# Kernel optimization log

Measured on AMD Instinct MI355X. Metric: run time of the kernel, lower is better.

## Reference

```python
import jax, jax.numpy as jnp
import numpy as np

FEATURES = 64
GROUPS = 8
KH = KW = 3
PAD = 1


def conv2d(x, w):
    # x: [B,C,H,W], w: [O,I,kh,kw], stride 1, padding 1
    return jax.lax.conv_general_dilated(
        x, w, window_strides=(1, 1), padding=((PAD, PAD), (PAD, PAD)),
        dimension_numbers=('NCHW', 'OIHW', 'NCHW'))


def _bilinear_gather(x, ys, xs):
    # x: [B,C,H,W]; ys, xs: [B,K,H,W] float sample coords. Zero outside bounds
    # (torchvision deform_conv2d convention).
    B, C, H, W = x.shape
    xf = x.reshape(B, C, H * W)
    y0 = jnp.floor(ys)
    x0 = jnp.floor(xs)
    dy = ys - y0
    dx = xs - x0

    def corner(yi, xi, w):
        valid = (yi >= 0) & (yi < H) & (xi >= 0) & (xi < W)
        yc = jnp.clip(yi, 0, H - 1).astype(jnp.int32)
        xc = jnp.clip(xi, 0, W - 1).astype(jnp.int32)
        idx = (yc * W + xc).reshape(B, -1)  # [B, K*H*W]
        g = jax.vmap(lambda xb, ib: xb[:, ib])(xf, idx)  # [B,C,K*H*W]
        g = g.reshape(B, C, *ys.shape[1:])  # [B,C,K,H,W]
        wm = jnp.where(valid, w, 0.0).astype(x.dtype)[:, None]
        return g * wm

    return (corner(y0, x0, (1 - dy) * (1 - dx))
            + corner(y0, x0 + 1, (1 - dy) * dx)
            + corner(y0 + 1, x0, dy * (1 - dx))
            + corner(y0 + 1, x0 + 1, dy * dx))


def deform_conv2d(x, offset, weight, bias, groups):
    # x: [B,C,H,W]; offset: [B,2*K,H,W] as (dy,dx) pairs per kernel tap;
    # weight: [Cout, Cin//groups, KH, KW]; bias: [Cout]. stride=1, pad=1, dil=1.
    B, C, H, W = x.shape
    Cout = weight.shape[0]
    K = KH * KW
    ky, kx = jnp.meshgrid(jnp.arange(KH), jnp.arange(KW), indexing='ij')
    ky = ky.reshape(K).astype(x.dtype)
    kx = kx.reshape(K).astype(x.dtype)
    off = offset.reshape(B, K, 2, H, W)
    ys = ((jnp.arange(H, dtype=x.dtype) - PAD)[None, None, :, None]
          + ky[None, :, None, None] + off[:, :, 0])  # [B,K,H,W]
    xs = ((jnp.arange(W, dtype=x.dtype) - PAD)[None, None, None, :]
          + kx[None, :, None, None] + off[:, :, 1])
    patches = _bilinear_gather(x, ys, xs)  # [B,C,K,H,W]
    p = patches.reshape(B, groups, C // groups, K, H, W)
    wg = weight.reshape(groups, Cout // groups, C // groups, K)
    out = jnp.einsum('bgikhw,goik->bgohw', p, wg).reshape(B, Cout, H, W)
    return out + bias[None, :, None, None]


def setup_inputs() -> dict:
    key = jax.random.key(0)
    ks = jax.random.split(key, 7)
    C = FEATURES
    x = jax.random.normal(ks[0], (8, C, 128, 128), dtype=jnp.float32)
    fan = C * KH * KW
    offset_w = jax.random.normal(ks[1], (2 * KH * KW, C, KH, KW), jnp.float32) / np.sqrt(fan)
    offset_b = jax.random.normal(ks[2], (2 * KH * KW,), jnp.float32) * 0.01
    prelu_a = jnp.full((1,), 0.25, dtype=jnp.float32)
    deconv_w = jax.random.normal(ks[3], (C, C // GROUPS, KH, KW), jnp.float32) / np.sqrt((C // GROUPS) * KH * KW)
    deconv_b = jax.random.normal(ks[4], (C,), jnp.float32) * 0.01
    conv_w = jax.random.normal(ks[5], (C, C, KH, KW), jnp.float32) / np.sqrt(fan)
    return {"x": x, "offset_w": offset_w, "offset_b": offset_b,
            "prelu_a": prelu_a, "deconv_w": deconv_w, "deconv_b": deconv_b,
            "conv_w": conv_w}


def reference(x, offset_w, offset_b, prelu_a, deconv_w, deconv_b, conv_w):
    residual = x
    o = conv2d(x, offset_w) + offset_b[None, :, None, None]
    offset = jnp.where(o >= 0, o, prelu_a[0] * o)          # PReLU(offset_conv1(x))
    feat = deform_conv2d(x, offset, deconv_w, deconv_b, GROUPS)
    atten = jax.nn.softmax(conv2d(x, conv_w), axis=-1)     # softmax over W
    return atten * feat + residual
```

## Files before the change

### kernel.cpp

```cpp
#include <hip/hip_runtime.h>
#include <math.h>

#define BB 8
#define C 64
#define H 128
#define W 128
#define KO 18
#define NG 8
#define CPG 8
#define KK 9
#define HW (H * W)
#define NCO 96
#define KTOT 576
#define AROW 72
#define PROW 72

typedef __bf16 bf16x8 __attribute__((ext_vector_type(8)));
typedef float f32x4 __attribute__((ext_vector_type(4)));
typedef unsigned int uint4v __attribute__((ext_vector_type(4)));

static __device__ __forceinline__ unsigned short f2bf(float f) {
    union { float f; unsigned u; } v; v.f = f;
    unsigned r = v.u + 0x7FFFu + ((v.u >> 16) & 1u);
    return (unsigned short)(r >> 16);
}

static __device__ __forceinline__ bf16x8 load_bf8(const unsigned short* p) {
    uint4v u = *(const uint4v*)p;
    return __builtin_bit_cast(bf16x8, u);
}
static __device__ __forceinline__ bf16x8 lds_bf8(const unsigned short* p) {
    uint4v u = *(const uint4v*)p;
    return __builtin_bit_cast(bf16x8, u);
}

static __device__ __forceinline__ float bflo(unsigned u) {
    union { unsigned u; float f; } v; v.u = u << 16; return v.f;
}
static __device__ __forceinline__ float bfhi(unsigned u) {
    union { unsigned u; float f; } v; v.u = u & 0xFFFF0000u; return v.f;
}

__global__ __launch_bounds__(256)
void xcl_prep_kernel(const float* __restrict__ x, unsigned short* __restrict__ xcl)
{
    const int lane = threadIdx.x & 63;
    const int cg = threadIdx.x >> 6;
    const size_t P = (size_t)blockIdx.x * 64 + lane;
    const int b = (int)(P >> 14);
    const int hw = (int)(P & 16383);

    union { unsigned short s[16]; uint4v v[2]; } u;
    const float* xp = x + ((size_t)b * C + cg * 16) * HW + hw;
#pragma unroll
    for (int i = 0; i < 16; i++)
        u.s[i] = f2bf(xp[i * HW]);

    uint4v* dst = (uint4v*)(xcl + P * 64 + cg * 16);
    dst[0] = u.v[0];
    dst[1] = u.v[1];
}

__global__ __launch_bounds__(256)
void wt_prep_kernel(const float* __restrict__ convw,
                    const float* __restrict__ offw,
                    unsigned short* __restrict__ wT)
{
    const int i = blockIdx.x * 256 + threadIdx.x;
    if (i >= NCO * KTOT) return;
    const int k = i % KTOT;
    const int co = i / KTOT;
    const int t = k >> 6;
    const int ci = k & 63;
    float v = 0.f;
    if (co < 64)       v = convw[((size_t)co * C + ci) * KK + t];
    else if (co < 82)  v = offw[((size_t)(co - 64) * C + ci) * KK + t];
    wT[i] = f2bf(v);
}

__global__ __launch_bounds__(256)
void awg_prep_kernel(const float* __restrict__ dw, unsigned short* __restrict__ awg)
{
    const int i = blockIdx.x * 256 + threadIdx.x;
    if (i >= KK * 2 * 32 * 32) return;
    const int ci = i & 31;
    const int row = (i >> 5) & 31;
    const int hf = (i >> 10) & 1;
    const int t = i >> 11;
    const int co = hf * 32 + row;
    const int cig = hf * 32 + ci;
    float v = 0.f;
    if ((co >> 3) == (cig >> 3))
        v = dw[((size_t)co * CPG + (cig & 7)) * KK + t];
    awg[i] = f2bf(v);
}

__global__ __launch_bounds__(256)
void conv_mfma_kernel(const unsigned short* __restrict__ xcl,
                      const unsigned short* __restrict__ wT,
                      const float* __restrict__ offb,
                      const float* __restrict__ prelu_a,
                      float* __restrict__ ws_offset,
                      float* __restrict__ ws_atten)
{
    __shared__ unsigned short aw[NCO * AROW];
    __shared__ float smax[4][2][64];
    __shared__ float ssum[4][2][64];

    const int lane = threadIdx.x & 63;
    const int q = __builtin_amdgcn_readfirstlane(threadIdx.x >> 6);
    const int m = lane & 15;
    const int qq = lane >> 4;
    const int hp = blockIdx.x & 63;
    const int b = blockIdx.x >> 6;
    const int h0 = hp * 2;

    f32x4 acc[4][6];
#pragma unroll
    for (int nt = 0; nt < 4; nt++)
#pragma unroll
        for (int mt = 0; mt < 6; mt++)
            acc[nt][mt] = (f32x4){0.f, 0.f, 0.f, 0.f};

    const int col0 = q * 32 + m;

#pragma unroll
    for (int t = 0; t < KK; t++) {
        const int dy = t / 3 - 1;
        const int dx = t % 3 - 1;

        bf16x8 bfr[2][4];
#pragma unroll
        for (int half = 0; half < 2; half++)
#pragma unroll
            for (int nt = 0; nt < 4; nt++) {
                const int y = h0 + (nt >> 1) + dy;
                const int xx = col0 + (nt & 1) * 16 + dx;
                const bool ok = (y >= 0) && (y < H) && (xx >= 0) && (xx < W);
                bf16x8 v = {};
                if (ok)
                    v = load_bf8(xcl + (((size_t)(b * H + y) * W + xx) * 64
                                        + half * 32 + qq * 8));
                bfr[half][nt] = v;
            }

        __syncthreads();
#pragma unroll
        for (int c = threadIdx.x; c < NCO * 8; c += 256) {
            const int row = c >> 3;
            const int col8 = (c & 7) * 8;
            *(uint4v*)(aw + row * AROW + col8) =
                *(const uint4v*)(wT + (size_t)row * KTOT + t * 64 + col8);
        }
        __syncthreads();

#pragma unroll
        for (int half = 0; half < 2; half++) {
#pragma unroll
            for (int mt = 0; mt < 6; mt++) {
                const bf16x8 afr = lds_bf8(
                    aw + (mt * 16 + m) * AROW + half * 32 + qq * 8);
#pragma unroll
                for (int nt = 0; nt < 4; nt++)
                    acc[nt][mt] = __builtin_amdgcn_mfma_f32_16x16x32_bf16(
                        afr, bfr[half][nt], acc[nt][mt], 0, 0, 0);
            }
        }
    }

    const float a = prelu_a[0];
#pragma unroll
    for (int nt = 0; nt < 4; nt++) {
        const int wrow = h0 + (nt >> 1);
        const int wcol = col0 + (nt & 1) * 16;
#pragma unroll
        for (int r = 0; r < 4; r++) {
            const int j = qq * 4 + r;
            float v = acc[nt][4][r] + offb[j];
            v = (v >= 0.f) ? v : a * v;
            ws_offset[((size_t)(b * KO + j)) * HW + wrow * W + wcol] = v;
        }
#pragma unroll
        for (int r = 0; r < 4; r++) {
            const int j = 16 + qq * 4 + r;
            if (j < KO) {
                float v = acc[nt][5][r] + offb[j];
                v = (v >= 0.f) ? v : a * v;
                ws_offset[((size_t)(b * KO + j)) * HW + wrow * W + wcol] = v;
            }
        }
    }

    float pm[2][4][4];
#pragma unroll
    for (int rr = 0; rr < 2; rr++)
#pragma unroll
        for (int mt = 0; mt < 4; mt++)
#pragma unroll
            for (int r = 0; r < 4; r++)
                pm[rr][mt][r] = fmaxf(acc[rr * 2][mt][r], acc[rr * 2 + 1][mt][r]);
#pragma unroll
    for (int off = 1; off < 16; off <<= 1)
#pragma unroll
        for (int rr = 0; rr < 2; rr++)
#pragma unroll
            for (int mt = 0; mt < 4; mt++)
#pragma unroll
                for (int r = 0; r < 4; r++)
                    pm[rr][mt][r] = fmaxf(pm[rr][mt][r],
                                          __shfl_xor(pm[rr][mt][r], off, 64));
    if (m == 0) {
#pragma unroll
        for (int rr = 0; rr < 2; rr++)
#pragma unroll
            for (int mt = 0; mt < 4; mt++)
#pragma unroll
                for (int r = 0; r < 4; r++)
                    smax[q][rr][mt * 16 + qq * 4 + r] = pm[rr][mt][r];
    }
    __syncthreads();

    float gm[2][4][4];
#pragma unroll
    for (int rr = 0; rr < 2; rr++)
#pragma unroll
        for (int mt = 0; mt < 4; mt++)
#pragma unroll
            for (int r = 0; r < 4; r++) {
                const int co = mt * 16 + qq * 4 + r;
                gm[rr][mt][r] = fmaxf(fmaxf(smax[0][rr][co], smax[1][rr][co]),
                                      fmaxf(smax[2][rr][co], smax[3][rr][co]));
            }
    float ps[2][4][4];
#pragma unroll
    for (int rr = 0; rr < 2; rr++)
#pragma unroll
        for (int mt = 0; mt < 4; mt++)
#pragma unroll
            for (int r = 0; r < 4; r++) {
                acc[rr * 2][mt][r] = __expf(acc[rr * 2][mt][r] - gm[rr][mt][r]);
                acc[rr * 2 + 1][mt][r] = __expf(acc[rr * 2 + 1][mt][r] - gm[rr][mt][r]);
                ps[rr][mt][r] = acc[rr * 2][mt][r] + acc[rr * 2 + 1][mt][r];
            }
#pragma unroll
    for (int off = 1; off < 16; off <<= 1)
#pragma unroll
        for (int rr = 0; rr < 2; rr++)
#pragma unroll
            for (int mt = 0; mt < 4; mt++)
#pragma unroll
                for (int r = 0; r < 4; r++)
                    ps[rr][mt][r] += __shfl_xor(ps[rr][mt][r], off, 64);
    if (m == 0) {
#pragma unroll
        for (int rr = 0; rr < 2; rr++)
#pragma unroll
            for (int mt = 0; mt < 4; mt++)
#pragma unroll
                for (int r = 0; r < 4; r++)
                    ssum[q][rr][mt * 16 + qq * 4 + r] = ps[rr][mt][r];
    }
    __syncthreads();

#pragma unroll
    for (int rr = 0; rr < 2; rr++)
#pragma unroll
        for (int mt = 0; mt < 4; mt++)
#pragma unroll
            for (int r = 0; r < 4; r++) {
                const int co = mt * 16 + qq * 4 + r;
                const float rinv = 1.f / (ssum[0][rr][co] + ssum[1][rr][co]
                                          + ssum[2][rr][co] + ssum[3][rr][co]);
                float* op = ws_atten + ((size_t)(b * 64 + co)) * HW
                            + (h0 + rr) * W;
                op[col0] = acc[rr * 2][mt][r] * rinv;
                op[col0 + 16] = acc[rr * 2 + 1][mt][r] * rinv;
            }
}

__global__ __launch_bounds__(256)
void deform_mfma_kernel(const float* __restrict__ x,
                        const unsigned short* __restrict__ xcl,
                        const unsigned short* __restrict__ awg,
                        const float* __restrict__ db,
                        const float* __restrict__ ws_offset,
                        const float* __restrict__ ws_atten,
                        float* __restrict__ out)
{
    __shared__ unsigned short Pl[4 * 2 * 16 * PROW];

    const int lane = threadIdx.x & 63;
    const int wv = __builtin_amdgcn_readfirstlane(threadIdx.x >> 6);

    const int b = blockIdx.x & 7;
    const int h = (blockIdx.x >> 3) & 127;
    const int halfrow = blockIdx.x >> 10;
    const int w0 = halfrow * 64 + wv * 16;

    const int pA = lane >> 3;
    const int pB = pA + 8;
    const int ch = lane & 7;

    const unsigned short* xclb = xcl + (size_t)b * HW * 64;
    const float* offbase = ws_offset + (size_t)b * KO * HW + h * W + w0;
    unsigned short* const Pw0 = Pl + (wv * 2 + 0) * 16 * PROW;
    unsigned short* const Pw1 = Pl + (wv * 2 + 1) * 16 * PROW;

    f32x4 acc[4];
#pragma unroll
    for (int i = 0; i < 4; i++) acc[i] = (f32x4){0.f, 0.f, 0.f, 0.f};

    float dyA = offbase[pA];
    float dxA = offbase[HW + pA];
    float dyB = offbase[pB];
    float dxB = offbase[HW + pB];

#pragma unroll
    for (int t = 0; t < KK; t++) {
        const int ky = t / 3;
        const int kx = t - ky * 3;

        float ndyA = 0.f, ndxA = 0.f, ndyB = 0.f, ndxB = 0.f;
        if (t + 1 < KK) {
            const float* ob2 = offbase + (size_t)(2 * t + 2) * HW;
            ndyA = ob2[pA];
            ndxA = ob2[HW + pA];
            ndyB = ob2[pB];
            ndxB = ob2[HW + pB];
        }

        float wa[4], wb[4];
        int oa[4], ob[4];
        {
            const float ys = (float)(h - 1 + ky) + dyA;
            const float xs = (float)(w0 + pA - 1 + kx) + dxA;
            const float y0f = floorf(ys), x0f = floorf(xs);
            const int y0 = (int)y0f, x0 = (int)x0f;
            const float fy = ys - y0f, fx = xs - x0f;
            const bool vy0 = (y0 >= 0) & (y0 < H), vy1 = (y0 + 1 >= 0) & (y0 + 1 < H);
            const bool vx0 = (x0 >= 0) & (x0 < W), vx1 = (x0 + 1 >= 0) & (x0 + 1 < W);
            wa[0] = (vy0 && vx0) ? (1.f - fy) * (1.f - fx) : 0.f;
            wa[1] = (vy0 && vx1) ? (1.f - fy) * fx : 0.f;
            wa[2] = (vy1 && vx0) ? fy * (1.f - fx) : 0.f;
            wa[3] = (vy1 && vx1) ? fy * fx : 0.f;
            const int yc0 = min(max(y0, 0), H - 1), yc1 = min(max(y0 + 1, 0), H - 1);
            const int xc0 = min(max(x0, 0), W - 1), xc1 = min(max(x0 + 1, 0), W - 1);
            oa[0] = (yc0 * W + xc0) * 64; oa[1] = (yc0 * W + xc1) * 64;
            oa[2] = (yc1 * W + xc0) * 64; oa[3] = (yc1 * W + xc1) * 64;
        }
        {
            const float ys = (float)(h - 1 + ky) + dyB;
            const float xs = (float)(w0 + pB - 1 + kx) + dxB;
            const float y0f = floorf(ys), x0f = floorf(xs);
            const int y0 = (int)y0f, x0 = (int)x0f;
            const float fy = ys - y0f, fx = xs - x0f;
            const bool vy0 = (y0 >= 0) & (y0 < H), vy1 = (y0 + 1 >= 0) & (y0 + 1 < H);
            const bool vx0 = (x0 >= 0) & (x0 < W), vx1 = (x0 + 1 >= 0) & (x0 + 1 < W);
            wb[0] = (vy0 && vx0) ? (1.f - fy) * (1.f - fx) : 0.f;
            wb[1] = (vy0 && vx1) ? (1.f - fy) * fx : 0.f;
            wb[2] = (vy1 && vx0) ? fy * (1.f - fx) : 0.f;
            wb[3] = (vy1 && vx1) ? fy * fx : 0.f;
            const int yc0 = min(max(y0, 0), H - 1), yc1 = min(max(y0 + 1, 0), H - 1);
            const int xc0 = min(max(x0, 0), W - 1), xc1 = min(max(x0 + 1, 0), W - 1);
            ob[0] = (yc0 * W + xc0) * 64; ob[1] = (yc0 * W + xc1) * 64;
            ob[2] = (yc1 * W + xc0) * 64; ob[3] = (yc1 * W + xc1) * 64;
        }

        uint4v rA[4], rB[4];
#pragma unroll
        for (int c = 0; c < 4; c++) {
            rA[c] = *(const uint4v*)(xclb + oa[c] + ch * 8);
            rB[c] = *(const uint4v*)(xclb + ob[c] + ch * 8);
        }

        unsigned short* const Pwt = (t & 1) ? Pw1 : Pw0;

        {
            bf16x8 pv;
#pragma unroll
            for (int d = 0; d < 4; d++) {
                const float lo = wa[0] * bflo(rA[0][d]) + wa[1] * bflo(rA[1][d])
                               + wa[2] * bflo(rA[2][d]) + wa[3] * bflo(rA[3][d]);
                const float hi = wa[0] * bfhi(rA[0][d]) + wa[1] * bfhi(rA[1][d])
                               + wa[2] * bfhi(rA[2][d]) + wa[3] * bfhi(rA[3][d]);
                pv[2 * d]     = (__bf16)lo;
                pv[2 * d + 1] = (__bf16)hi;
            }
            *(bf16x8*)(Pwt + pA * PROW + ch * 8) = pv;
        }
        {
            bf16x8 pv;
#pragma unroll
            for (int d = 0; d < 4; d++) {
                const float lo = wb[0] * bflo(rB[0][d]) + wb[1] * bflo(rB[1][d])
                               + wb[2] * bflo(rB[2][d]) + wb[3] * bflo(rB[3][d]);
                const float hi = wb[0] * bfhi(rB[0][d]) + wb[1] * bfhi(rB[1][d])
                               + wb[2] * bfhi(rB[2][d]) + wb[3] * bfhi(rB[3][d]);
                pv[2 * d]     = (__bf16)lo;
                pv[2 * d + 1] = (__bf16)hi;
            }
            *(bf16x8*)(Pwt + pB * PROW + ch * 8) = pv;
        }

        asm volatile("s_waitcnt lgkmcnt(0)" ::: "memory");

        const int m = lane & 15;
        const int qq = lane >> 4;
#pragma unroll
        for (int hf = 0; hf < 2; hf++) {
            const bf16x8 bfr = lds_bf8(Pwt + m * PROW + hf * 32 + qq * 8);
#pragma unroll
            for (int mtl = 0; mtl < 2; mtl++) {
                const bf16x8 afr = load_bf8(
                    awg + ((size_t)((t * 2 + hf) * 32 + mtl * 16 + m)) * 32 + qq * 8);
                acc[hf * 2 + mtl] = __builtin_amdgcn_mfma_f32_16x16x32_bf16(
                    afr, bfr, acc[hf * 2 + mtl], 0, 0, 0);
            }
        }

        dyA = ndyA; dxA = ndxA; dyB = ndyB; dxB = ndxB;
    }

    const int n = lane & 15;
    const int qq = lane >> 4;
    const float* attp = ws_atten + (size_t)b * C * HW + h * W + w0 + n;
    const float* xr = x + (size_t)b * C * HW + h * W + w0 + n;
    float* op = out + (size_t)b * C * HW + h * W + w0 + n;
#pragma unroll
    for (int a = 0; a < 4; a++)
#pragma unroll
        for (int r = 0; r < 4; r++) {
            const int co = a * 16 + qq * 4 + r;
            const float f = acc[a][r] + db[co];
            op[(size_t)co * HW] = attp[(size_t)co * HW] * f + xr[(size_t)co * HW];
        }
}

extern "C" void kernel_launch(void* const* d_in, const int* in_sizes, int n_in,
                              void* d_out, int out_size, void* d_ws, size_t ws_size,
                              hipStream_t stream) {
    const float* x        = (const float*)d_in[0];
    const float* offset_w = (const float*)d_in[1];
    const float* offset_b = (const float*)d_in[2];
    const float* prelu_a  = (const float*)d_in[3];
    const float* deconv_w = (const float*)d_in[4];
    const float* deconv_b = (const float*)d_in[5];
    const float* conv_w   = (const float*)d_in[6];
    float* out = (float*)d_out;

    float* ws_offset = (float*)d_ws;
    float* ws_atten  = ws_offset + (size_t)BB * KO * HW;
    unsigned short* xcl = (unsigned short*)(ws_atten + (size_t)BB * C * HW);
    unsigned short* wT  = xcl + (size_t)BB * HW * C;
    unsigned short* awg = wT + (size_t)NCO * KTOT;

    xcl_prep_kernel<<<dim3((BB * HW) / 64), dim3(256), 0, stream>>>(x, xcl);
    wt_prep_kernel<<<dim3((NCO * KTOT + 255) / 256), dim3(256), 0, stream>>>(
        conv_w, offset_w, wT);
    awg_prep_kernel<<<dim3((KK * 2 * 32 * 32 + 255) / 256), dim3(256), 0, stream>>>(
        deconv_w, awg);

    conv_mfma_kernel<<<dim3(BB * H / 2), dim3(256), 0, stream>>>(
        xcl, wT, offset_b, prelu_a, ws_offset, ws_atten);

    deform_mfma_kernel<<<dim3(BB * H * 2), dim3(256), 0, stream>>>(
        x, xcl, awg, deconv_b, ws_offset, ws_atten, out);
}
```

Before: 184.0 us.

## Merge prep kernels into one launch and give conv blocks one row each

The three preprocessing kernels are folded into a single launch that picks its branch by block index, removing two kernel launches. The conv MFMA kernel now handles one output row per block instead of two, doubling the grid to 1024 blocks and halving the accumulator registers. This aims to raise occupancy and parallelism. In exchange, each weight tile copied into LDS is reused over half as many pixels, so weight traffic and barrier overhead per output grow.

```diff
diff --git a/kernel.cpp b/kernel.cpp
--- a/kernel.cpp
+++ b/kernel.cpp
@@ -15,6 +15,10 @@
 #define AROW 72
 #define PROW 72
 
+#define NB_XCL (BB * HW / 64)
+#define NB_WT  (NCO * KTOT / 256)
+#define NB_AWG (KK * 2 * 32 * 32 / 256)
+
 typedef __bf16 bf16x8 __attribute__((ext_vector_type(8)));
 typedef float f32x4 __attribute__((ext_vector_type(4)));
 typedef unsigned int uint4v __attribute__((ext_vector_type(4)));
@@ -42,57 +46,54 @@
 }
 
 __global__ __launch_bounds__(256)
-void xcl_prep_kernel(const float* __restrict__ x, unsigned short* __restrict__ xcl)
+void prep_kernel(const float* __restrict__ x,
+                 const float* __restrict__ convw,
+                 const float* __restrict__ offw,
+                 const float* __restrict__ dw,
+                 unsigned short* __restrict__ xcl,
+                 unsigned short* __restrict__ wT,
+                 unsigned short* __restrict__ awg)
 {
-    const int lane = threadIdx.x & 63;
-    const int cg = threadIdx.x >> 6;
-    const size_t P = (size_t)blockIdx.x * 64 + lane;
-    const int b = (int)(P >> 14);
-    const int hw = (int)(P & 16383);
-
-    union { unsigned short s[16]; uint4v v[2]; } u;
-    const float* xp = x + ((size_t)b * C + cg * 16) * HW + hw;
-#pragma unroll
-    for (int i = 0; i < 16; i++)
-        u.s[i] = f2bf(xp[i * HW]);
-
-    uint4v* dst = (uint4v*)(xcl + P * 64 + cg * 16);
-    dst[0] = u.v[0];
-    dst[1] = u.v[1];
-}
-
-__global__ __launch_bounds__(256)
-void wt_prep_kernel(const float* __restrict__ convw,
-                    const float* __restrict__ offw,
-                    unsigned short* __restrict__ wT)
-{
-    const int i = blockIdx.x * 256 + threadIdx.x;
-    if (i >= NCO * KTOT) return;
-    const int k = i % KTOT;
-    const int co = i / KTOT;
-    const int t = k >> 6;
-    const int ci = k & 63;
-    float v = 0.f;
-    if (co < 64)       v = convw[((size_t)co * C + ci) * KK + t];
-    else if (co < 82)  v = offw[((size_t)(co - 64) * C + ci) * KK + t];
-    wT[i] = f2bf(v);
-}
-
-__global__ __launch_bounds__(256)
-void awg_prep_kernel(const float* __restrict__ dw, unsigned short* __restrict__ awg)
-{
-    const int i = blockIdx.x * 256 + threadIdx.x;
-    if (i >= KK * 2 * 32 * 32) return;
-    const int ci = i & 31;
-    const int row = (i >> 5) & 31;
-    const int hf = (i >> 10) & 1;
-    const int t = i >> 11;
-    const int co = hf * 32 + row;
-    const int cig = hf * 32 + ci;
-    float v = 0.f;
-    if ((co >> 3) == (cig >> 3))
-        v = dw[((size_t)co * CPG + (cig & 7)) * KK + t];
-    awg[i] = f2bf(v);
+    const int blk = blockIdx.x;
+    if (blk < NB_XCL) {
+        const int lane = threadIdx.x & 63;
+        const int cg = threadIdx.x >> 6;
+        const size_t P = (size_t)blk * 64 + lane;
+        const int b = (int)(P >> 14);
+        const int hw = (int)(P & 16383);
+
+        union { unsigned short s[16]; uint4v v[2]; } u;
+        const float* xp = x + ((size_t)b * C + cg * 16) * HW + hw;
+#pragma unroll
+        for (int i = 0; i < 16; i++)
+            u.s[i] = f2bf(xp[i * HW]);
+
+        uint4v* dst = (uint4v*)(xcl + P * 64 + cg * 16);
+        dst[0] = u.v[0];
+        dst[1] = u.v[1];
+    } else if (blk < NB_XCL + NB_WT) {
+        const int i = (blk - NB_XCL) * 256 + threadIdx.x;
+        const int k = i % KTOT;
+        const int co = i / KTOT;
+        const int t = k >> 6;
+        const int ci = k & 63;
+        float v = 0.f;
+        if (co < 64)       v = convw[((size_t)co * C + ci) * KK + t];
+        else if (co < 82)  v = offw[((size_t)(co - 64) * C + ci) * KK + t];
+        wT[i] = f2bf(v);
+    } else {
+        const int i = (blk - NB_XCL - NB_WT) * 256 + threadIdx.x;
+        const int ci = i & 31;
+        const int row = (i >> 5) & 31;
+        const int hf = (i >> 10) & 1;
+        const int t = i >> 11;
+        const int co = hf * 32 + row;
+        const int cig = hf * 32 + ci;
+        float v = 0.f;
+        if ((co >> 3) == (cig >> 3))
+            v = dw[((size_t)co * CPG + (cig & 7)) * KK + t];
+        awg[i] = f2bf(v);
+    }
 }
 
 __global__ __launch_bounds__(256)
@@ -104,20 +105,19 @@
                       float* __restrict__ ws_atten)
 {
     __shared__ unsigned short aw[NCO * AROW];
-    __shared__ float smax[4][2][64];
-    __shared__ float ssum[4][2][64];
+    __shared__ float smax[4][64];
+    __shared__ float ssum[4][64];
 
     const int lane = threadIdx.x & 63;
     const int q = __builtin_amdgcn_readfirstlane(threadIdx.x >> 6);
     const int m = lane & 15;
     const int qq = lane >> 4;
-    const int hp = blockIdx.x & 63;
-    const int b = blockIdx.x >> 6;
-    const int h0 = hp * 2;
-
-    f32x4 acc[4][6];
-#pragma unroll
-    for (int nt = 0; nt < 4; nt++)
+    const int h = blockIdx.x & 127;
+    const int b = blockIdx.x >> 7;
+
+    f32x4 acc[2][6];
+#pragma unroll
+    for (int nt = 0; nt < 2; nt++)
 #pragma unroll
         for (int mt = 0; mt < 6; mt++)
             acc[nt][mt] = (f32x4){0.f, 0.f, 0.f, 0.f};
@@ -129,14 +129,15 @@
         const int dy = t / 3 - 1;
         const int dx = t % 3 - 1;
 
-        bf16x8 bfr[2][4];
+        bf16x8 bfr[2][2];
+        const int y = h + dy;
+        const bool oky = (y >= 0) && (y < H);
 #pragma unroll
         for (int half = 0; half < 2; half++)
 #pragma unroll
-            for (int nt = 0; nt < 4; nt++) {
-                const int y = h0 + (nt >> 1) + dy;
-                const int xx = col0 + (nt & 1) * 16 + dx;
-                const bool ok = (y >= 0) && (y < H) && (xx >= 0) && (xx < W);
+            for (int nt = 0; nt < 2; nt++) {
+                const int xx = col0 + nt * 16 + dx;
+                const bool ok = oky && (xx >= 0) && (xx < W);
                 bf16x8 v = {};
                 if (ok)
                     v = load_bf8(xcl + (((size_t)(b * H + y) * W + xx) * 64
@@ -161,7 +162,7 @@
                 const bf16x8 afr = lds_bf8(
                     aw + (mt * 16 + m) * AROW + half * 32 + qq * 8);
 #pragma unroll
-                for (int nt = 0; nt < 4; nt++)
+                for (int nt = 0; nt < 2; nt++)
                     acc[nt][mt] = __builtin_amdgcn_mfma_f32_16x16x32_bf16(
                         afr, bfr[half][nt], acc[nt][mt], 0, 0, 0);
             }
@@ -170,15 +171,14 @@
 
     const float a = prelu_a[0];
 #pragma unroll
-    for (int nt = 0; nt < 4; nt++) {
-        const int wrow = h0 + (nt >> 1);
-        const int wcol = col0 + (nt & 1) * 16;
+    for (int nt = 0; nt < 2; nt++) {
+        const int wcol = col0 + nt * 16;
 #pragma unroll
         for (int r = 0; r < 4; r++) {
             const int j = qq * 4 + r;
             float v = acc[nt][4][r] + offb[j];
             v = (v >= 0.f) ? v : a * v;
-            ws_offset[((size_t)(b * KO + j)) * HW + wrow * W + wcol] = v;
+            ws_offset[((size_t)(b * KO + j)) * HW + h * W + wcol] = v;
         }
 #pragma unroll
         for (int r = 0; r < 4; r++) {
@@ -186,96 +186,78 @@
             if (j < KO) {
                 float v = acc[nt][5][r] + offb[j];
                 v = (v >= 0.f) ? v : a * v;
-                ws_offset[((size_t)(b * KO + j)) * HW + wrow * W + wcol] = v;
-            }
-        }
-    }
-
-    float pm[2][4][4];
-#pragma unroll
-    for (int rr = 0; rr < 2; rr++)
+                ws_offset[((size_t)(b * KO + j)) * HW + h * W + wcol] = v;
+            }
+        }
+    }
+
+    float pm[4][4];
+#pragma unroll
+    for (int mt = 0; mt < 4; mt++)
+#pragma unroll
+        for (int r = 0; r < 4; r++)
+            pm[mt][r] = fmaxf(acc[0][mt][r], acc[1][mt][r]);
+#pragma unroll
+    for (int off = 1; off < 16; off <<= 1)
 #pragma unroll
         for (int mt = 0; mt < 4; mt++)
 #pragma unroll
             for (int r = 0; r < 4; r++)
-                pm[rr][mt][r] = fmaxf(acc[rr * 2][mt][r], acc[rr * 2 + 1][mt][r]);
+                pm[mt][r] = fmaxf(pm[mt][r], __shfl_xor(pm[mt][r], off, 64));
+    if (m == 0) {
+#pragma unroll
+        for (int mt = 0; mt < 4; mt++)
+#pragma unroll
+            for (int r = 0; r < 4; r++)
+                smax[q][mt * 16 + qq * 4 + r] = pm[mt][r];
+    }
+    __syncthreads();
+
+    float gm[4][4];
+#pragma unroll
+    for (int mt = 0; mt < 4; mt++)
+#pragma unroll
+        for (int r = 0; r < 4; r++) {
+            const int co = mt * 16 + qq * 4 + r;
+            gm[mt][r] = fmaxf(fmaxf(smax[0][co], smax[1][co]),
+                              fmaxf(smax[2][co], smax[3][co]));
+        }
+    float ps[4][4];
+#pragma unroll
+    for (int mt = 0; mt < 4; mt++)
+#pragma unroll
+        for (int r = 0; r < 4; r++) {
+            acc[0][mt][r] = __expf(acc[0][mt][r] - gm[mt][r]);
+            acc[1][mt][r] = __expf(acc[1][mt][r] - gm[mt][r]);
+            ps[mt][r] = acc[0][mt][r] + acc[1][mt][r];
+        }
 #pragma unroll
     for (int off = 1; off < 16; off <<= 1)
 #pragma unroll
-        for (int rr = 0; rr < 2; rr++)
-#pragma unroll
-            for (int mt = 0; mt < 4; mt++)
-#pragma unroll
-                for (int r = 0; r < 4; r++)
-                    pm[rr][mt][r] = fmaxf(pm[rr][mt][r],
-                                          __shfl_xor(pm[rr][mt][r], off, 64));
+        for (int mt = 0; mt < 4; mt++)
+#pragma unroll
+            for (int r = 0; r < 4; r++)
+                ps[mt][r] += __shfl_xor(ps[mt][r], off, 64);
     if (m == 0) {
 #pragma unroll
-        for (int rr = 0; rr < 2; rr++)
-#pragma unroll
-            for (int mt = 0; mt < 4; mt++)
-#pragma unroll
-                for (int r = 0; r < 4; r++)
-                    smax[q][rr][mt * 16 + qq * 4 + r] = pm[rr][mt][r];
+        for (int mt = 0; mt < 4; mt++)
+#pragma unroll
+            for (int r = 0; r < 4; r++)
+                ssum[q][mt * 16 + qq * 4 + r] = ps[mt][r];
     }
     __syncthreads();
 
-    float gm[2][4][4];
-#pragma unroll
-    for (int rr = 0; rr < 2; rr++)
-#pragma unroll
-        for (int mt = 0; mt < 4; mt++)
-#pragma unroll
-            for (int r = 0; r < 4; r++) {
-                const int co = mt * 16 + qq * 4 + r;
-                gm[rr][mt][r] = fmaxf(fmaxf(smax[0][rr][co], smax[1][rr][co]),
-                                      fmaxf(smax[2][rr][co], smax[3][rr][co]));
-            }
-    float ps[2][4][4];
-#pragma unroll
-    for (int rr = 0; rr < 2; rr++)
-#pragma unroll
-        for (int mt = 0; mt < 4; mt++)
-#pragma unroll
-            for (int r = 0; r < 4; r++) {
-                acc[rr * 2][mt][r] = __expf(acc[rr * 2][mt][r] - gm[rr][mt][r]);
-                acc[rr * 2 + 1][mt][r] = __expf(acc[rr * 2 + 1][mt][r] - gm[rr][mt][r]);
-                ps[rr][mt][r] = acc[rr * 2][mt][r] + acc[rr * 2 + 1][mt][r];
-            }
-#pragma unroll
-    for (int off = 1; off < 16; off <<= 1)
-#pragma unroll
-        for (int rr = 0; rr < 2; rr++)
-#pragma unroll
-            for (int mt = 0; mt < 4; mt++)
-#pragma unroll
-                for (int r = 0; r < 4; r++)
-                    ps[rr][mt][r] += __shfl_xor(ps[rr][mt][r], off, 64);
-    if (m == 0) {
-#pragma unroll
-        for (int rr = 0; rr < 2; rr++)
-#pragma unroll
-            for (int mt = 0; mt < 4; mt++)
-#pragma unroll
-                for (int r = 0; r < 4; r++)
-                    ssum[q][rr][mt * 16 + qq * 4 + r] = ps[rr][mt][r];
-    }
-    __syncthreads();
-
-#pragma unroll
-    for (int rr = 0; rr < 2; rr++)
-#pragma unroll
-        for (int mt = 0; mt < 4; mt++)
-#pragma unroll
-            for (int r = 0; r < 4; r++) {
-                const int co = mt * 16 + qq * 4 + r;
-                const float rinv = 1.f / (ssum[0][rr][co] + ssum[1][rr][co]
-                                          + ssum[2][rr][co] + ssum[3][rr][co]);
-                float* op = ws_atten + ((size_t)(b * 64 + co)) * HW
-                            + (h0 + rr) * W;
-                op[col0] = acc[rr * 2][mt][r] * rinv;
-                op[col0 + 16] = acc[rr * 2 + 1][mt][r] * rinv;
-            }
+#pragma unroll
+    for (int mt = 0; mt < 4; mt++)
+#pragma unroll
+        for (int r = 0; r < 4; r++) {
+            const int co = mt * 16 + qq * 4 + r;
+            const float rinv = 1.f / (ssum[0][co] + ssum[1][co]
+                                      + ssum[2][co] + ssum[3][co]);
+            float* op = ws_atten + ((size_t)(b * 64 + co)) * HW + h * W;
+            op[col0] = acc[0][mt][r] * rinv;
+            op[col0 + 16] = acc[1][mt][r] * rinv;
+        }
 }
 
 __global__ __launch_bounds__(256)
@@ -454,13 +436,10 @@
     unsigned short* wT  = xcl + (size_t)BB * HW * C;
     unsigned short* awg = wT + (size_t)NCO * KTOT;
 
-    xcl_prep_kernel<<<dim3((BB * HW) / 64), dim3(256), 0, stream>>>(x, xcl);
-    wt_prep_kernel<<<dim3((NCO * KTOT + 255) / 256), dim3(256), 0, stream>>>(
-        conv_w, offset_w, wT);
-    awg_prep_kernel<<<dim3((KK * 2 * 32 * 32 + 255) / 256), dim3(256), 0, stream>>>(
-        deconv_w, awg);
-
-    conv_mfma_kernel<<<dim3(BB * H / 2), dim3(256), 0, stream>>>(
+    prep_kernel<<<dim3(NB_XCL + NB_WT + NB_AWG), dim3(256), 0, stream>>>(
+        x, conv_w, offset_w, deconv_w, xcl, wT, awg);
+
+    conv_mfma_kernel<<<dim3(BB * H), dim3(256), 0, stream>>>(
         xcl, wT, offset_b, prelu_a, ws_offset, ws_atten);
 
     deform_mfma_kernel<<<dim3(BB * H * 2), dim3(256), 0, stream>>>(
```

Result: slower. 188.4 us (+2.4%).

## Fuse prep kernels and load MFMA A-fragments directly from pre-swizzled weights

Applied to the files above, without the earlier changes.

Merges the three preprocessing kernels (x to channels-last bf16, conv weight transpose, grouped deform weight expansion) into one launch that dispatches on block index. The conv weights are now written in a fragment-ready layout, so the conv kernel reads each MFMA A operand as one contiguous 16-byte global load instead of staging weights through LDS with two barriers per tap. This removes two kernel launches and the per-tap LDS copy and synchronisation. In exchange each wave reloads weights from global memory/L2 rather than sharing them through LDS.

```diff
diff --git a/kernel.cpp b/kernel.cpp
--- a/kernel.cpp
+++ b/kernel.cpp
@@ -12,8 +12,11 @@
 #define HW (H * W)
 #define NCO 96
 #define KTOT 576
-#define AROW 72
 #define PROW 72
+
+#define NB_XCL (BB * HW / 64)
+#define NB_WT  (NCO * KTOT / 256)
+#define NB_AWG (KK * 2 * 32 * 32 / 256)
 
 typedef __bf16 bf16x8 __attribute__((ext_vector_type(8)));
 typedef float f32x4 __attribute__((ext_vector_type(4)));
@@ -42,68 +45,67 @@
 }
 
 __global__ __launch_bounds__(256)
-void xcl_prep_kernel(const float* __restrict__ x, unsigned short* __restrict__ xcl)
+void prep_kernel(const float* __restrict__ x,
+                 const float* __restrict__ convw,
+                 const float* __restrict__ offw,
+                 const float* __restrict__ dw,
+                 unsigned short* __restrict__ xcl,
+                 unsigned short* __restrict__ wTT,
+                 unsigned short* __restrict__ awg)
 {
-    const int lane = threadIdx.x & 63;
-    const int cg = threadIdx.x >> 6;
-    const size_t P = (size_t)blockIdx.x * 64 + lane;
-    const int b = (int)(P >> 14);
-    const int hw = (int)(P & 16383);
-
-    union { unsigned short s[16]; uint4v v[2]; } u;
-    const float* xp = x + ((size_t)b * C + cg * 16) * HW + hw;
-#pragma unroll
-    for (int i = 0; i < 16; i++)
-        u.s[i] = f2bf(xp[i * HW]);
-
-    uint4v* dst = (uint4v*)(xcl + P * 64 + cg * 16);
-    dst[0] = u.v[0];
-    dst[1] = u.v[1];
-}
-
-__global__ __launch_bounds__(256)
-void wt_prep_kernel(const float* __restrict__ convw,
-                    const float* __restrict__ offw,
-                    unsigned short* __restrict__ wT)
-{
-    const int i = blockIdx.x * 256 + threadIdx.x;
-    if (i >= NCO * KTOT) return;
-    const int k = i % KTOT;
-    const int co = i / KTOT;
-    const int t = k >> 6;
-    const int ci = k & 63;
-    float v = 0.f;
-    if (co < 64)       v = convw[((size_t)co * C + ci) * KK + t];
-    else if (co < 82)  v = offw[((size_t)(co - 64) * C + ci) * KK + t];
-    wT[i] = f2bf(v);
-}
-
-__global__ __launch_bounds__(256)
-void awg_prep_kernel(const float* __restrict__ dw, unsigned short* __restrict__ awg)
-{
-    const int i = blockIdx.x * 256 + threadIdx.x;
-    if (i >= KK * 2 * 32 * 32) return;
-    const int ci = i & 31;
-    const int row = (i >> 5) & 31;
-    const int hf = (i >> 10) & 1;
-    const int t = i >> 11;
-    const int co = hf * 32 + row;
-    const int cig = hf * 32 + ci;
-    float v = 0.f;
-    if ((co >> 3) == (cig >> 3))
-        v = dw[((size_t)co * CPG + (cig & 7)) * KK + t];
-    awg[i] = f2bf(v);
+    const int blk = blockIdx.x;
+    if (blk < NB_XCL) {
+        const int lane = threadIdx.x & 63;
+        const int cg = threadIdx.x >> 6;
+        const size_t P = (size_t)blk * 64 + lane;
+        const int b = (int)(P >> 14);
+        const int hw = (int)(P & 16383);
+
+        union { unsigned short s[16]; uint4v v[2]; } u;
+        const float* xp = x + ((size_t)b * C + cg * 16) * HW + hw;
+#pragma unroll
+        for (int i = 0; i < 16; i++)
+            u.s[i] = f2bf(xp[i * HW]);
+
+        uint4v* dst = (uint4v*)(xcl + P * 64 + cg * 16);
+        dst[0] = u.v[0];
+        dst[1] = u.v[1];
+    } else if (blk < NB_XCL + NB_WT) {
+        const int i = (blk - NB_XCL) * 256 + threadIdx.x;
+        const int e = i & 7;
+        const int row = (i >> 3) % 96;
+        const int g = i / 768;
+        const int qq = g & 3;
+        const int half = (g >> 2) & 1;
+        const int t = g >> 3;
+        const int ci = half * 32 + qq * 8 + e;
+        float v = 0.f;
+        if (row < 64)       v = convw[((size_t)row * C + ci) * KK + t];
+        else if (row < 82)  v = offw[((size_t)(row - 64) * C + ci) * KK + t];
+        wTT[i] = f2bf(v);
+    } else {
+        const int i = (blk - NB_XCL - NB_WT) * 256 + threadIdx.x;
+        const int ci = i & 31;
+        const int row = (i >> 5) & 31;
+        const int hf = (i >> 10) & 1;
+        const int t = i >> 11;
+        const int co = hf * 32 + row;
+        const int cig = hf * 32 + ci;
+        float v = 0.f;
+        if ((co >> 3) == (cig >> 3))
+            v = dw[((size_t)co * CPG + (cig & 7)) * KK + t];
+        awg[i] = f2bf(v);
+    }
 }
 
 __global__ __launch_bounds__(256)
 void conv_mfma_kernel(const unsigned short* __restrict__ xcl,
-                      const unsigned short* __restrict__ wT,
+                      const unsigned short* __restrict__ wTT,
                       const float* __restrict__ offb,
                       const float* __restrict__ prelu_a,
                       float* __restrict__ ws_offset,
                       float* __restrict__ ws_atten)
 {
-    __shared__ unsigned short aw[NCO * AROW];
     __shared__ float smax[4][2][64];
     __shared__ float ssum[4][2][64];
 
@@ -123,6 +125,7 @@
             acc[nt][mt] = (f32x4){0.f, 0.f, 0.f, 0.f};
 
     const int col0 = q * 32 + m;
+    const unsigned short* wA = wTT + ((size_t)qq * 96 + m) * 8;
 
 #pragma unroll
     for (int t = 0; t < KK; t++) {
@@ -144,22 +147,12 @@
                 bfr[half][nt] = v;
             }
 
-        __syncthreads();
-#pragma unroll
-        for (int c = threadIdx.x; c < NCO * 8; c += 256) {
-            const int row = c >> 3;
-            const int col8 = (c & 7) * 8;
-            *(uint4v*)(aw + row * AROW + col8) =
-                *(const uint4v*)(wT + (size_t)row * KTOT + t * 64 + col8);
-        }
-        __syncthreads();
-
 #pragma unroll
         for (int half = 0; half < 2; half++) {
 #pragma unroll
             for (int mt = 0; mt < 6; mt++) {
-                const bf16x8 afr = lds_bf8(
-                    aw + (mt * 16 + m) * AROW + half * 32 + qq * 8);
+                const bf16x8 afr = load_bf8(
+                    wA + ((size_t)((t * 2 + half) * 4) * 96 + mt * 16) * 8);
 #pragma unroll
                 for (int nt = 0; nt < 4; nt++)
                     acc[nt][mt] = __builtin_amdgcn_mfma_f32_16x16x32_bf16(
@@ -451,17 +444,14 @@
     float* ws_offset = (float*)d_ws;
     float* ws_atten  = ws_offset + (size_t)BB * KO * HW;
     unsigned short* xcl = (unsigned short*)(ws_atten + (size_t)BB * C * HW);
-    unsigned short* wT  = xcl + (size_t)BB * HW * C;
-    unsigned short* awg = wT + (size_t)NCO * KTOT;
-
-    xcl_prep_kernel<<<dim3((BB * HW) / 64), dim3(256), 0, stream>>>(x, xcl);
-    wt_prep_kernel<<<dim3((NCO * KTOT + 255) / 256), dim3(256), 0, stream>>>(
-        conv_w, offset_w, wT);
-    awg_prep_kernel<<<dim3((KK * 2 * 32 * 32 + 255) / 256), dim3(256), 0, stream>>>(
-        deconv_w, awg);
+    unsigned short* wTT = xcl + (size_t)BB * HW * C;
+    unsigned short* awg = wTT + (size_t)NCO * KTOT;
+
+    prep_kernel<<<dim3(NB_XCL + NB_WT + NB_AWG), dim3(256), 0, stream>>>(
+        x, conv_w, offset_w, deconv_w, xcl, wTT, awg);
 
     conv_mfma_kernel<<<dim3(BB * H / 2), dim3(256), 0, stream>>>(
-        xcl, wT, offset_b, prelu_a, ws_offset, ws_atten);
+        xcl, wTT, offset_b, prelu_a, ws_offset, ws_atten);
 
     deform_mfma_kernel<<<dim3(BB * H * 2), dim3(256), 0, stream>>>(
         x, xcl, awg, deconv_b, ws_offset, ws_atten, out);
```

Result: slower. 201.3 us (+9.4%).

## Merge prep kernels and double-buffer weight/input staging in conv MFMA loop

Applied to the files above, without the earlier changes.

Folds the three preprocessing kernels into a single launch that dispatches on block index, which removes two kernel launches. In the conv MFMA kernel, weight taps are now staged into a double-buffered LDS array and the next tap's input fragments are prefetched into registers while the current tap's MFMAs run. This cuts the per-tap barriers from two to one. It also adds launch_bounds occupancy hint 2, at the cost of more registers for the prefetch buffers and double the LDS for weights.

```diff
diff --git a/kernel.cpp b/kernel.cpp
--- a/kernel.cpp
+++ b/kernel.cpp
@@ -15,6 +15,10 @@
 #define AROW 72
 #define PROW 72
 
+#define NB_XCL (BB * HW / 64)
+#define NB_WT  (NCO * KTOT / 256)
+#define NB_AWG (KK * 2 * 32 * 32 / 256)
+
 typedef __bf16 bf16x8 __attribute__((ext_vector_type(8)));
 typedef float f32x4 __attribute__((ext_vector_type(4)));
 typedef unsigned int uint4v __attribute__((ext_vector_type(4)));
@@ -42,60 +46,91 @@
 }
 
 __global__ __launch_bounds__(256)
-void xcl_prep_kernel(const float* __restrict__ x, unsigned short* __restrict__ xcl)
+void prep_kernel(const float* __restrict__ x,
+                 const float* __restrict__ convw,
+                 const float* __restrict__ offw,
+                 const float* __restrict__ dw,
+                 unsigned short* __restrict__ xcl,
+                 unsigned short* __restrict__ wT,
+                 unsigned short* __restrict__ awg)
 {
-    const int lane = threadIdx.x & 63;
-    const int cg = threadIdx.x >> 6;
-    const size_t P = (size_t)blockIdx.x * 64 + lane;
-    const int b = (int)(P >> 14);
-    const int hw = (int)(P & 16383);
-
-    union { unsigned short s[16]; uint4v v[2]; } u;
-    const float* xp = x + ((size_t)b * C + cg * 16) * HW + hw;
-#pragma unroll
-    for (int i = 0; i < 16; i++)
-        u.s[i] = f2bf(xp[i * HW]);
-
-    uint4v* dst = (uint4v*)(xcl + P * 64 + cg * 16);
-    dst[0] = u.v[0];
-    dst[1] = u.v[1];
-}
-
-__global__ __launch_bounds__(256)
-void wt_prep_kernel(const float* __restrict__ convw,
-                    const float* __restrict__ offw,
-                    unsigned short* __restrict__ wT)
+    const int blk = blockIdx.x;
+    if (blk < NB_XCL) {
+        const int lane = threadIdx.x & 63;
+        const int cg = threadIdx.x >> 6;
+        const size_t P = (size_t)blk * 64 + lane;
+        const int b = (int)(P >> 14);
+        const int hw = (int)(P & 16383);
+
+        union { unsigned short s[16]; uint4v v[2]; } u;
+        const float* xp = x + ((size_t)b * C + cg * 16) * HW + hw;
+#pragma unroll
+        for (int i = 0; i < 16; i++)
+            u.s[i] = f2bf(xp[i * HW]);
+
+        uint4v* dst = (uint4v*)(xcl + P * 64 + cg * 16);
+        dst[0] = u.v[0];
+        dst[1] = u.v[1];
+    } else if (blk < NB_XCL + NB_WT) {
+        const int i = (blk - NB_XCL) * 256 + threadIdx.x;
+        const int k = i % KTOT;
+        const int co = i / KTOT;
+        const int t = k >> 6;
+        const int ci = k & 63;
+        float v = 0.f;
+        if (co < 64)       v = convw[((size_t)co * C + ci) * KK + t];
+        else if (co < 82)  v = offw[((size_t)(co - 64) * C + ci) * KK + t];
+        wT[i] = f2bf(v);
+    } else {
+        const int i = (blk - NB_XCL - NB_WT) * 256 + threadIdx.x;
+        const int ci = i & 31;
+        const int row = (i >> 5) & 31;
+        const int hf = (i >> 10) & 1;
+        const int t = i >> 11;
+        const int co = hf * 32 + row;
+        const int cig = hf * 32 + ci;
+        float v = 0.f;
+        if ((co >> 3) == (cig >> 3))
+            v = dw[((size_t)co * CPG + (cig & 7)) * KK + t];
+        awg[i] = f2bf(v);
+    }
+}
+
+static __device__ __forceinline__ void stage_tap(
+    const unsigned short* __restrict__ wT, unsigned short* __restrict__ dst,
+    int t, int tid)
 {
-    const int i = blockIdx.x * 256 + threadIdx.x;
-    if (i >= NCO * KTOT) return;
-    const int k = i % KTOT;
-    const int co = i / KTOT;
-    const int t = k >> 6;
-    const int ci = k & 63;
-    float v = 0.f;
-    if (co < 64)       v = convw[((size_t)co * C + ci) * KK + t];
-    else if (co < 82)  v = offw[((size_t)(co - 64) * C + ci) * KK + t];
-    wT[i] = f2bf(v);
-}
-
-__global__ __launch_bounds__(256)
-void awg_prep_kernel(const float* __restrict__ dw, unsigned short* __restrict__ awg)
+#pragma unroll
+    for (int c = tid; c < NCO * 8; c += 256) {
+        const int row = c >> 3;
+        const int col8 = (c & 7) * 8;
+        *(uint4v*)(dst + row * AROW + col8) =
+            *(const uint4v*)(wT + (size_t)row * KTOT + t * 64 + col8);
+    }
+}
+
+static __device__ __forceinline__ void load_b(
+    const unsigned short* __restrict__ xcl, int b, int h0, int col0, int qq,
+    int t, bf16x8 (&dst)[2][4])
 {
-    const int i = blockIdx.x * 256 + threadIdx.x;
-    if (i >= KK * 2 * 32 * 32) return;
-    const int ci = i & 31;
-    const int row = (i >> 5) & 31;
-    const int hf = (i >> 10) & 1;
-    const int t = i >> 11;
-    const int co = hf * 32 + row;
-    const int cig = hf * 32 + ci;
-    float v = 0.f;
-    if ((co >> 3) == (cig >> 3))
-        v = dw[((size_t)co * CPG + (cig & 7)) * KK + t];
-    awg[i] = f2bf(v);
-}
-
-__global__ __launch_bounds__(256)
+    const int dy = t / 3 - 1;
+    const int dx = t % 3 - 1;
+#pragma unroll
+    for (int half = 0; half < 2; half++)
+#pragma unroll
+        for (int nt = 0; nt < 4; nt++) {
+            const int y = h0 + (nt >> 1) + dy;
+            const int xx = col0 + (nt & 1) * 16 + dx;
+            const bool ok = (y >= 0) && (y < H) && (xx >= 0) && (xx < W);
+            bf16x8 v = {};
+            if (ok)
+                v = load_bf8(xcl + (((size_t)(b * H + y) * W + xx) * 64
+                                    + half * 32 + qq * 8));
+            dst[half][nt] = v;
+        }
+}
+
+__global__ __launch_bounds__(256, 2)
 void conv_mfma_kernel(const unsigned short* __restrict__ xcl,
                       const unsigned short* __restrict__ wT,
                       const float* __restrict__ offb,
@@ -103,7 +138,7 @@
                       float* __restrict__ ws_offset,
                       float* __restrict__ ws_atten)
 {
-    __shared__ unsigned short aw[NCO * AROW];
+    __shared__ unsigned short aw[2][NCO * AROW];
     __shared__ float smax[4][2][64];
     __shared__ float ssum[4][2][64];
 
@@ -124,48 +159,37 @@
 
     const int col0 = q * 32 + m;
 
+    bf16x8 bcur[2][4], bnxt[2][4];
+    stage_tap(wT, aw[0], 0, threadIdx.x);
+    load_b(xcl, b, h0, col0, qq, 0, bcur);
+    __syncthreads();
+
 #pragma unroll
     for (int t = 0; t < KK; t++) {
-        const int dy = t / 3 - 1;
-        const int dx = t % 3 - 1;
-
-        bf16x8 bfr[2][4];
-#pragma unroll
-        for (int half = 0; half < 2; half++)
-#pragma unroll
-            for (int nt = 0; nt < 4; nt++) {
-                const int y = h0 + (nt >> 1) + dy;
-                const int xx = col0 + (nt & 1) * 16 + dx;
-                const bool ok = (y >= 0) && (y < H) && (xx >= 0) && (xx < W);
-                bf16x8 v = {};
-                if (ok)
-                    v = load_bf8(xcl + (((size_t)(b * H + y) * W + xx) * 64
-                                        + half * 32 + qq * 8));
-                bfr[half][nt] = v;
-            }
-
-        __syncthreads();
-#pragma unroll
-        for (int c = threadIdx.x; c < NCO * 8; c += 256) {
-            const int row = c >> 3;
-            const int col8 = (c & 7) * 8;
-            *(uint4v*)(aw + row * AROW + col8) =
-                *(const uint4v*)(wT + (size_t)row * KTOT + t * 64 + col8);
-        }
-        __syncthreads();
+        if (t + 1 < KK) {
+            stage_tap(wT, aw[(t + 1) & 1], t + 1, threadIdx.x);
+            load_b(xcl, b, h0, col0, qq, t + 1, bnxt);
+        }
 
 #pragma unroll
         for (int half = 0; half < 2; half++) {
 #pragma unroll
             for (int mt = 0; mt < 6; mt++) {
                 const bf16x8 afr = lds_bf8(
-                    aw + (mt * 16 + m) * AROW + half * 32 + qq * 8);
+                    &aw[t & 1][(mt * 16 + m) * AROW + half * 32 + qq * 8]);
 #pragma unroll
                 for (int nt = 0; nt < 4; nt++)
                     acc[nt][mt] = __builtin_amdgcn_mfma_f32_16x16x32_bf16(
-                        afr, bfr[half][nt], acc[nt][mt], 0, 0, 0);
-            }
-        }
+                        afr, bcur[half][nt], acc[nt][mt], 0, 0, 0);
+            }
+        }
+        __syncthreads();
+
+#pragma unroll
+        for (int half = 0; half < 2; half++)
+#pragma unroll
+            for (int nt = 0; nt < 4; nt++)
+                bcur[half][nt] = bnxt[half][nt];
     }
 
     const float a = prelu_a[0];
@@ -454,11 +478,8 @@
     unsigned short* wT  = xcl + (size_t)BB * HW * C;
     unsigned short* awg = wT + (size_t)NCO * KTOT;
 
-    xcl_prep_kernel<<<dim3((BB * HW) / 64), dim3(256), 0, stream>>>(x, xcl);
-    wt_prep_kernel<<<dim3((NCO * KTOT + 255) / 256), dim3(256), 0, stream>>>(
-        conv_w, offset_w, wT);
-    awg_prep_kernel<<<dim3((KK * 2 * 32 * 32 + 255) / 256), dim3(256), 0, stream>>>(
-        deconv_w, awg);
+    prep_kernel<<<dim3(NB_XCL + NB_WT + NB_AWG), dim3(256), 0, stream>>>(
+        x, conv_w, offset_w, deconv_w, xcl, wT, awg);
 
     conv_mfma_kernel<<<dim3(BB * H / 2), dim3(256), 0, stream>>>(
         xcl, wT, offset_b, prelu_a, ws_offset, ws_atten);
```

New measurement: 177.9 us. -3.3%, faster.
